# Performance work log

Measured on AMD Instinct MI355X. Metric: run time of the kernel, lower is better.

## Reference

```python
import jax, jax.numpy as jnp
import numpy as np

N, E, L, D, H = 20000, 100000, 4, 64, 8
HID = H * D  # LSTM hidden size = num_heads * out_dim


def setup_inputs() -> dict:
    key = jax.random.key(0)
    ks = jax.random.split(key, 8)
    s = 0.05
    return {
        "features": jax.random.normal(ks[0], (N, D), jnp.float32),
        "type_mask": jax.random.randint(ks[1], (N,), 0, 3),
        "edge_metapath_indices": jax.random.randint(ks[2], (E, L), 0, N),
        "dst": jax.random.randint(ks[3], (E,), 0, N),
        "W_ih": jax.random.normal(ks[4], (4 * HID, D), jnp.float32) * s,
        "W_hh": jax.random.normal(ks[5], (4 * HID, HID), jnp.float32) * s,
        "b_ih": jnp.zeros((4 * HID,), jnp.float32),
        "b_hh": jnp.zeros((4 * HID,), jnp.float32),
        "attn1_w": jax.random.normal(ks[6], (H, D), jnp.float32) * s,
        "attn2": jax.random.normal(ks[7], (1, H, D), jnp.float32) * s,
    }


def _lstm_last_hidden(x, W_ih, W_hh, b_ih, b_hh):
    # x: [L, E, D] time-major. PyTorch LSTM gate order: i, f, g, o.
    h0 = jnp.zeros((x.shape[1], W_hh.shape[1]), x.dtype)
    b = b_ih + b_hh

    def step(carry, xt):
        h, c = carry
        gates = xt @ W_ih.T + h @ W_hh.T + b  # [E, 4*HID]
        i, f, g, o = jnp.split(gates, 4, axis=-1)
        c = jax.nn.sigmoid(f) * c + jax.nn.sigmoid(i) * jnp.tanh(g)
        h = jax.nn.sigmoid(o) * jnp.tanh(c)
        return (h, c), None

    (h, _), _ = jax.lax.scan(step, (h0, h0), x)
    return h  # [E, HID]


def reference(features, type_mask, edge_metapath_indices, dst,
              W_ih, W_hh, b_ih, b_hh, attn1_w, attn2):
    alpha = 0.01  # LeakyReLU slope
    # gather metapath node features: [E, L, D]
    edata = features[edge_metapath_indices]
    h = _lstm_last_hidden(jnp.swapaxes(edata, 0, 1), W_ih, W_hh, b_ih, b_hh)
    eft = h.reshape(-1, H, D)  # [E, H, D]
    center = features[edge_metapath_indices[:, -1]]  # [E, D]
    a1 = center @ attn1_w.T                      # [E, H]
    a2 = jnp.sum(eft * attn2, axis=-1)           # [E, H]
    a = jax.nn.leaky_relu(a1 + a2, negative_slope=alpha)[:, :, None]  # [E, H, 1]
    # edge softmax: segmented by destination node
    amax = jax.ops.segment_max(a, dst, num_segments=N)
    amax = jnp.where(jnp.isfinite(amax), amax, 0.0)
    ex = jnp.exp(a - amax[dst])
    denom = jax.ops.segment_sum(ex, dst, num_segments=N)
    attn = ex / denom[dst]  # every edge's segment is nonempty
    # message passing: scatter-sum of eft * attn into dst nodes
    return jax.ops.segment_sum(eft * attn, dst, num_segments=N)  # [N, H, D]
```

## Files before the change

### kernel.cpp

```cpp
#include <hip/hip_runtime.h>
#include <hip/hip_bf16.h>
#include <stdint.h>

#define N_NODES 20000
#define E_EDGES 100000
#define L_SEQ   4
#define D_FEAT  64
#define H_HEADS 8
#define HID     512

typedef __attribute__((ext_vector_type(8))) short short8;
typedef __attribute__((ext_vector_type(4))) float floatx4;

__device__ __forceinline__ float sigmoidf_(float x) { return 1.0f / (1.0f + __expf(-x)); }
__device__ __forceinline__ float tanhf_(float x) {
    x = fminf(15.f, fmaxf(-15.f, x));
    float e = __expf(2.f * x);
    return (e - 1.f) / (e + 1.f);
}
__device__ __forceinline__ unsigned fkey(float f) {
    unsigned u = __float_as_uint(f);
    return (u & 0x80000000u) ? ~u : (u | 0x80000000u);
}
__device__ __forceinline__ float fdecode(unsigned k) {
    if (k == 0u) return 0.0f;
    unsigned u = (k & 0x80000000u) ? (k ^ 0x80000000u) : ~k;
    return __uint_as_float(u);
}
__device__ __forceinline__ short f2bf(float x) {
    __hip_bfloat16 b = __float2bfloat16(x);
    return *(short*)&b;
}
__device__ __forceinline__ float bf2f(short x) {
    __hip_bfloat16 b = *(__hip_bfloat16*)&x;
    return __bfloat162float(b);
}

__device__ __forceinline__ void gload16(const void* g, const void* l) {
    __builtin_amdgcn_global_load_lds(
        (const __attribute__((address_space(1))) unsigned int*)(uintptr_t)g,
        (__attribute__((address_space(3))) unsigned int*)(unsigned int)(uintptr_t)l,
        16, 0, 0);
}

__global__ __launch_bounds__(256) void feat2bf16(const float* __restrict__ f, short* __restrict__ fb) {
    int i = blockIdx.x * 256 + threadIdx.x;
    if (i < N_NODES * D_FEAT) fb[i] = f2bf(f[i]);
}

__global__ __launch_bounds__(128) void convert_weights(
    const float* __restrict__ W_ih, const float* __restrict__ W_hh,
    const float* __restrict__ b_ih, const float* __restrict__ b_hh,
    short* __restrict__ Wb_ih, short* __restrict__ Wb_hh, float* __restrict__ bias)
{
    int rp = blockIdx.x;
    int hblock = rp >> 7, rem = rp & 127;
    int half = (rem >> 6) & 1, gate = (rem >> 4) & 3, j = rem & 15;
    int ro = gate * HID + hblock * 32 + half * 16 + j;
    for (int k = threadIdx.x; k < D_FEAT; k += 128)
        Wb_ih[rp * D_FEAT + k] = f2bf(W_ih[ro * D_FEAT + k]);
    for (int k = threadIdx.x; k < HID; k += 128)
        Wb_hh[rp * HID + k] = f2bf(W_hh[ro * HID + k]);
    if (threadIdx.x == 0) bias[ro] = b_ih[ro] + b_hh[ro];
}

template <int FIRST>
__global__ __launch_bounds__(256) void lstm_mfma(
    const short* __restrict__ feats_bf,
    const int*   __restrict__ mp,
    const short* __restrict__ Wb_ih,
    const short* __restrict__ Wb_hh,
    const float* __restrict__ bias,
    const short* __restrict__ h_prev,
    short*       __restrict__ h_next,
    short*       __restrict__ c_state,
    int t, int cnt, int nslices)
{
    __shared__ __align__(16) short At[128 * 64];
    __shared__ __align__(16) short Bt[128 * 64];

    const int b     = blockIdx.x;
    const int xcd   = b & 7;
    const int slot  = b >> 3;
    const int g     = slot >> 4;
    const int bn    = slot & 15;
    const int slice = g * 8 + xcd;
    if (slice >= nslices) return;
    const int e0    = slice * 128;
    const int hb    = bn * 32;

    const int tid   = threadIdx.x;
    const int lane  = tid & 63;
    const int w     = tid >> 6;
    const int waveM = w & 1;
    const int waveN = w >> 1;
    const int quad  = lane >> 4;
    const int c16   = lane & 15;

    floatx4 acc[4][4];
#pragma unroll
    for (int a = 0; a < 4; ++a)
#pragma unroll
        for (int bb = 0; bb < 4; ++bb) acc[a][bb] = (floatx4){0.f, 0.f, 0.f, 0.f};

    const int nch = FIRST ? 1 : 9;
    for (int kc = 0; kc < nch; ++kc) {
#pragma unroll
        for (int i = 0; i < 4; ++i) {
            int sb = w * 256 + i * 64;
            int s  = sb + lane;
            int m  = s >> 3, p = s & 7;
            int pg = p ^ (m & 7);
            int e = e0 + m; if (e >= cnt) e = cnt - 1;
            const void* ga;
            if (kc == 0) {
                int row = mp[e * L_SEQ + t];
                ga = (const void*)(feats_bf + row * D_FEAT + pg * 8);
            } else {
                ga = (const void*)(h_prev + (size_t)e * HID + (kc - 1) * 64 + pg * 8);
            }
            gload16(ga, (const void*)&At[sb * 8]);
            int r = bn * 128 + m;
            const void* gb = (kc == 0)
                ? (const void*)(Wb_ih + r * D_FEAT + pg * 8)
                : (const void*)(Wb_hh + (size_t)r * HID + (kc - 1) * 64 + pg * 8);
            gload16(gb, (const void*)&Bt[sb * 8]);
        }
        __syncthreads();

#pragma unroll
        for (int ks = 0; ks < 2; ++ks) {
            short8 af[4], bfv[4];
#pragma unroll
            for (int mf = 0; mf < 4; ++mf) {
                int m  = waveM * 64 + mf * 16 + c16;
                int pw = ks * 4 + quad;
                af[mf] = *(const short8*)&At[m * 64 + ((pw ^ (m & 7)) * 8)];
            }
#pragma unroll
            for (int nf = 0; nf < 4; ++nf) {
                int n  = waveN * 64 + nf * 16 + c16;
                int pw = ks * 4 + quad;
                bfv[nf] = *(const short8*)&Bt[n * 64 + ((pw ^ (n & 7)) * 8)];
            }
#pragma unroll
            for (int mf = 0; mf < 4; ++mf)
#pragma unroll
                for (int nf = 0; nf < 4; ++nf)
                    acc[mf][nf] = __builtin_amdgcn_mfma_f32_16x16x32_bf16(
                        af[mf], bfv[nf], acc[mf][nf], 0, 0, 0);
        }
        __syncthreads();
    }

    const int n = hb + waveN * 16 + c16;
    const float bi  = bias[n];
    const float bff = bias[HID + n];
    const float bg  = bias[2 * HID + n];
    const float bo  = bias[3 * HID + n];
#pragma unroll
    for (int mf = 0; mf < 4; ++mf) {
#pragma unroll
        for (int r = 0; r < 4; ++r) {
            int e = e0 + waveM * 64 + mf * 16 + quad * 4 + r;
            if (e < cnt) {
                float gi = acc[mf][0][r] + bi;
                float gf = acc[mf][1][r] + bff;
                float gg = acc[mf][2][r] + bg;
                float go = acc[mf][3][r] + bo;
                float c_old = FIRST ? 0.f : bf2f(c_state[(size_t)e * HID + n]);
                float cn = sigmoidf_(gf) * c_old + sigmoidf_(gi) * tanhf_(gg);
                c_state[(size_t)e * HID + n] = f2bf(cn);
                h_next[(size_t)e * HID + n] = f2bf(sigmoidf_(go) * tanhf_(cn));
            }
        }
    }
}

__global__ __launch_bounds__(256) void attn_logits(
    const float* __restrict__ features,
    const int*   __restrict__ mp,
    const __hip_bfloat16* __restrict__ hfin,
    const float* __restrict__ attn1_w,
    const float* __restrict__ attn2,
    const int*   __restrict__ dst,
    float*       __restrict__ a_out,
    unsigned*    __restrict__ amax_key)
{
    const int e    = blockIdx.x * 4 + (threadIdx.x >> 6);
    const int lane = threadIdx.x & 63;
    const int ctr  = mp[e * L_SEQ + (L_SEQ - 1)];
    const float cd = features[ctr * D_FEAT + lane];
    const int dn   = dst[e];
#pragma unroll
    for (int h = 0; h < H_HEADS; ++h) {
        float v = cd * attn1_w[h * D_FEAT + lane]
                + __bfloat162float(hfin[(size_t)e * HID + h * D_FEAT + lane]) * attn2[h * D_FEAT + lane];
#pragma unroll
        for (int off = 32; off; off >>= 1) v += __shfl_xor(v, off, 64);
        if (lane == 0) {
            float lv = v > 0.f ? v : 0.01f * v;
            a_out[e * H_HEADS + h] = lv;
            atomicMax(&amax_key[dn * H_HEADS + h], fkey(lv));
        }
    }
}

__global__ __launch_bounds__(256) void exp_denom(
    const int*      __restrict__ dst,
    float*          __restrict__ a_out,
    const unsigned* __restrict__ amax_key,
    float*          __restrict__ denom)
{
    int i = blockIdx.x * 256 + threadIdx.x;
    if (i >= E_EDGES * H_HEADS) return;
    int e = i >> 3, h = i & 7;
    int dn = dst[e];
    float am = fdecode(amax_key[dn * H_HEADS + h]);
    float ex = __expf(a_out[i] - am);
    a_out[i] = ex;
    atomicAdd(&denom[dn * H_HEADS + h], ex);
}

__global__ __launch_bounds__(256) void scatter_out(
    const int*   __restrict__ dst,
    const float* __restrict__ a_out,
    const float* __restrict__ denom,
    const __hip_bfloat16* __restrict__ hfin,
    float*       __restrict__ out)
{
    const int e  = blockIdx.x;
    const int dn = dst[e];
    for (int j = threadIdx.x; j < HID; j += 256) {
        int h = j >> 6;
        float wgt = a_out[e * H_HEADS + h] / denom[dn * H_HEADS + h];
        atomicAdd(&out[(size_t)dn * HID + j], __bfloat162float(hfin[(size_t)e * HID + j]) * wgt);
    }
}

extern "C" void kernel_launch(void* const* d_in, const int* in_sizes, int n_in,
                              void* d_out, int out_size, void* d_ws, size_t ws_size,
                              hipStream_t stream) {
    const float* features = (const float*)d_in[0];
    const int*   mp       = (const int*)d_in[2];
    const int*   dst      = (const int*)d_in[3];
    const float* W_ih     = (const float*)d_in[4];
    const float* W_hh     = (const float*)d_in[5];
    const float* b_ih     = (const float*)d_in[6];
    const float* b_hh     = (const float*)d_in[7];
    const float* attn1_w  = (const float*)d_in[8];
    const float* attn2    = (const float*)d_in[9];
    float* out = (float*)d_out;

    char* ws = (char*)d_ws;
    size_t off = 0;
    float*    a_scr    = (float*)(ws + off); off += (size_t)E_EDGES * H_HEADS * sizeof(float);
    float*    denom    = (float*)(ws + off); off += (size_t)N_NODES * H_HEADS * sizeof(float);
    unsigned* amax_key = (unsigned*)(ws + off); off += (size_t)N_NODES * H_HEADS * sizeof(unsigned);
    short*    feats_bf = (short*)(ws + off); off += (size_t)N_NODES * D_FEAT * sizeof(short);
    short*    Wb_ih    = (short*)(ws + off); off += (size_t)4 * HID * D_FEAT * sizeof(short);
    short*    Wb_hh    = (short*)(ws + off); off += (size_t)4 * HID * HID * sizeof(short);
    float*    bias     = (float*)(ws + off); off += (size_t)4 * HID * sizeof(float);
    off = (off + 255) & ~(size_t)255;
    short*    eft      = (short*)(ws + off); off += (size_t)E_EDGES * HID * sizeof(short);
    off = (off + 255) & ~(size_t)255;

    const size_t per_edge = (size_t)HID * (2 + 2 + 2);
    size_t avail = (ws_size > off) ? (ws_size - off) : 0;
    long long cs_ll = ((long long)(avail / per_edge) / 1024) * 1024;
    int cs = (int)(cs_ll < 1024 ? 1024 : (cs_ll > E_EDGES ? E_EDGES : cs_ll));

    short* hA = (short*)(ws + off);
    short* hB = hA + (size_t)cs * HID;
    short* cS = hB + (size_t)cs * HID;

    hipMemsetAsync(d_out, 0, (size_t)out_size * sizeof(float), stream);
    hipMemsetAsync(denom, 0, (size_t)N_NODES * H_HEADS * sizeof(float), stream);
    hipMemsetAsync(amax_key, 0, (size_t)N_NODES * H_HEADS * sizeof(unsigned), stream);

    feat2bf16<<<(N_NODES * D_FEAT + 255) / 256, 256, 0, stream>>>(features, feats_bf);
    convert_weights<<<4 * HID, 128, 0, stream>>>(W_ih, W_hh, b_ih, b_hh, Wb_ih, Wb_hh, bias);

    for (int e0 = 0; e0 < E_EDGES; e0 += cs) {
        int cnt = E_EDGES - e0 < cs ? E_EDGES - e0 : cs;
        int nslices = (cnt + 127) / 128;
        int nslices_pad = (nslices + 7) & ~7;
        int nblk = nslices_pad * 16;
        const int* mpc = mp + (size_t)e0 * L_SEQ;
        short* eft_c = eft + (size_t)e0 * HID;
        lstm_mfma<1><<<nblk, 256, 0, stream>>>(feats_bf, mpc, Wb_ih, Wb_hh, bias, hA, hA, cS, 0, cnt, nslices);
        lstm_mfma<0><<<nblk, 256, 0, stream>>>(feats_bf, mpc, Wb_ih, Wb_hh, bias, hA, hB, cS, 1, cnt, nslices);
        lstm_mfma<0><<<nblk, 256, 0, stream>>>(feats_bf, mpc, Wb_ih, Wb_hh, bias, hB, hA, cS, 2, cnt, nslices);
        lstm_mfma<0><<<nblk, 256, 0, stream>>>(feats_bf, mpc, Wb_ih, Wb_hh, bias, hA, eft_c, cS, 3, cnt, nslices);
    }

    attn_logits<<<E_EDGES / 4, 256, 0, stream>>>(features, mp, (const __hip_bfloat16*)eft,
                                                 attn1_w, attn2, dst, a_scr, amax_key);
    exp_denom<<<(E_EDGES * H_HEADS + 255) / 256, 256, 0, stream>>>(dst, a_scr, amax_key, denom);
    scatter_out<<<E_EDGES, 256, 0, stream>>>(dst, a_scr, denom, (const __hip_bfloat16*)eft, out);
}
```

Measured before the change: 1.530 ms.

## Replace atomic edge-softmax scatter with CSR-based per-node gather

Builds a CSR index of edges grouped by destination (histogram, single-block scan, atomic fill), then computes the segment max, denominator and weighted sum per node in one gather kernel, dropping the global atomicMax/atomicAdd scatter passes and the output memset. The LSTM kernel is also restructured to hoist per-lane address computation and separate the input-projection chunk from the recurrent chunks with pointer increments. The CSR build adds several small serial launches, including a single-block scan, and edge order within a node is nondeterministic.

```diff
diff --git a/kernel.cpp b/kernel.cpp
--- a/kernel.cpp
+++ b/kernel.cpp
@@ -64,6 +64,47 @@
     if (threadIdx.x == 0) bias[ro] = b_ih[ro] + b_hh[ro];
 }
 
+__global__ __launch_bounds__(256) void deg_hist(const int* __restrict__ dst, int* __restrict__ deg) {
+    int i = blockIdx.x * 256 + threadIdx.x;
+    if (i < E_EDGES) atomicAdd(&deg[dst[i]], 1);
+}
+
+__global__ __launch_bounds__(1024) void scan_deg(const int* __restrict__ deg,
+                                                 int* __restrict__ row, int* __restrict__ cursor) {
+    __shared__ int buf[1024];
+    __shared__ int s_carry;
+    const int tid = threadIdx.x;
+    if (tid == 0) s_carry = 0;
+    __syncthreads();
+    for (int base = 0; base < N_NODES; base += 1024) {
+        int idx = base + tid;
+        int v = (idx < N_NODES) ? deg[idx] : 0;
+        buf[tid] = v;
+        __syncthreads();
+        for (int offd = 1; offd < 1024; offd <<= 1) {
+            int tv = (tid >= offd) ? buf[tid - offd] : 0;
+            __syncthreads();
+            buf[tid] += tv;
+            __syncthreads();
+        }
+        int c0 = s_carry;
+        if (idx < N_NODES) { row[idx] = c0 + buf[tid] - v; cursor[idx] = c0 + buf[tid] - v; }
+        __syncthreads();
+        if (tid == 1023) s_carry = c0 + buf[1023];
+        __syncthreads();
+    }
+    if (tid == 0) row[N_NODES] = s_carry;
+}
+
+__global__ __launch_bounds__(256) void fill_csr(const int* __restrict__ dst,
+                                                int* __restrict__ cursor, int* __restrict__ elist) {
+    int i = blockIdx.x * 256 + threadIdx.x;
+    if (i < E_EDGES) {
+        int p = atomicAdd(&cursor[dst[i]], 1);
+        elist[p] = i;
+    }
+}
+
 template <int FIRST>
 __global__ __launch_bounds__(256) void lstm_mfma(
     const short* __restrict__ feats_bf,
@@ -103,31 +144,18 @@
 #pragma unroll
         for (int bb = 0; bb < 4; ++bb) acc[a][bb] = (floatx4){0.f, 0.f, 0.f, 0.f};
 
-    const int nch = FIRST ? 1 : 9;
-    for (int kc = 0; kc < nch; ++kc) {
-#pragma unroll
-        for (int i = 0; i < 4; ++i) {
-            int sb = w * 256 + i * 64;
-            int s  = sb + lane;
-            int m  = s >> 3, p = s & 7;
-            int pg = p ^ (m & 7);
-            int e = e0 + m; if (e >= cnt) e = cnt - 1;
-            const void* ga;
-            if (kc == 0) {
-                int row = mp[e * L_SEQ + t];
-                ga = (const void*)(feats_bf + row * D_FEAT + pg * 8);
-            } else {
-                ga = (const void*)(h_prev + (size_t)e * HID + (kc - 1) * 64 + pg * 8);
-            }
-            gload16(ga, (const void*)&At[sb * 8]);
-            int r = bn * 128 + m;
-            const void* gb = (kc == 0)
-                ? (const void*)(Wb_ih + r * D_FEAT + pg * 8)
-                : (const void*)(Wb_hh + (size_t)r * HID + (kc - 1) * 64 + pg * 8);
-            gload16(gb, (const void*)&Bt[sb * 8]);
-        }
-        __syncthreads();
-
+    int eidx[4], mm[4], pgo[4];
+#pragma unroll
+    for (int i = 0; i < 4; ++i) {
+        int s = w * 256 + i * 64 + lane;
+        int m = s >> 3, p = s & 7;
+        pgo[i] = p ^ (m & 7);
+        mm[i]  = m;
+        int e  = e0 + m; if (e >= cnt) e = cnt - 1;
+        eidx[i] = e;
+    }
+
+    auto compute = [&]() {
 #pragma unroll
         for (int ks = 0; ks < 2; ++ks) {
             short8 af[4], bfv[4];
@@ -150,7 +178,37 @@
                     acc[mf][nf] = __builtin_amdgcn_mfma_f32_16x16x32_bf16(
                         af[mf], bfv[nf], acc[mf][nf], 0, 0, 0);
         }
-        __syncthreads();
+    };
+
+#pragma unroll
+    for (int i = 0; i < 4; ++i) {
+        int sb = w * 256 + i * 64;
+        int rowf = mp[eidx[i] * L_SEQ + t];
+        gload16((const void*)(feats_bf + rowf * D_FEAT + pgo[i] * 8), (const void*)&At[sb * 8]);
+        gload16((const void*)(Wb_ih + (bn * 128 + mm[i]) * D_FEAT + pgo[i] * 8), (const void*)&Bt[sb * 8]);
+    }
+    __syncthreads();
+    compute();
+
+    if (!FIRST) {
+        const short* ah[4]; const short* bh[4];
+#pragma unroll
+        for (int i = 0; i < 4; ++i) {
+            ah[i] = h_prev + (size_t)eidx[i] * HID + pgo[i] * 8;
+            bh[i] = Wb_hh + (size_t)(bn * 128 + mm[i]) * HID + pgo[i] * 8;
+        }
+        for (int kc = 1; kc <= 8; ++kc) {
+            __syncthreads();
+#pragma unroll
+            for (int i = 0; i < 4; ++i) {
+                int sb = w * 256 + i * 64;
+                gload16((const void*)ah[i], (const void*)&At[sb * 8]);
+                gload16((const void*)bh[i], (const void*)&Bt[sb * 8]);
+                ah[i] += 64; bh[i] += 64;
+            }
+            __syncthreads();
+            compute();
+        }
     }
 
     const int n = hb + waveN * 16 + c16;
@@ -183,15 +241,12 @@
     const __hip_bfloat16* __restrict__ hfin,
     const float* __restrict__ attn1_w,
     const float* __restrict__ attn2,
-    const int*   __restrict__ dst,
-    float*       __restrict__ a_out,
-    unsigned*    __restrict__ amax_key)
+    float*       __restrict__ a_out)
 {
     const int e    = blockIdx.x * 4 + (threadIdx.x >> 6);
     const int lane = threadIdx.x & 63;
     const int ctr  = mp[e * L_SEQ + (L_SEQ - 1)];
     const float cd = features[ctr * D_FEAT + lane];
-    const int dn   = dst[e];
 #pragma unroll
     for (int h = 0; h < H_HEADS; ++h) {
         float v = cd * attn1_w[h * D_FEAT + lane]
@@ -201,41 +256,70 @@
         if (lane == 0) {
             float lv = v > 0.f ? v : 0.01f * v;
             a_out[e * H_HEADS + h] = lv;
-            atomicMax(&amax_key[dn * H_HEADS + h], fkey(lv));
-        }
-    }
-}
-
-__global__ __launch_bounds__(256) void exp_denom(
-    const int*      __restrict__ dst,
-    float*          __restrict__ a_out,
-    const unsigned* __restrict__ amax_key,
-    float*          __restrict__ denom)
-{
-    int i = blockIdx.x * 256 + threadIdx.x;
-    if (i >= E_EDGES * H_HEADS) return;
-    int e = i >> 3, h = i & 7;
-    int dn = dst[e];
-    float am = fdecode(amax_key[dn * H_HEADS + h]);
-    float ex = __expf(a_out[i] - am);
-    a_out[i] = ex;
-    atomicAdd(&denom[dn * H_HEADS + h], ex);
-}
-
-__global__ __launch_bounds__(256) void scatter_out(
-    const int*   __restrict__ dst,
-    const float* __restrict__ a_out,
-    const float* __restrict__ denom,
-    const __hip_bfloat16* __restrict__ hfin,
+        }
+    }
+}
+
+__global__ __launch_bounds__(256) void gather_out(
+    const int*   __restrict__ row,
+    const int*   __restrict__ elist,
+    const float* __restrict__ a_scr,
+    const short* __restrict__ eft,
     float*       __restrict__ out)
 {
-    const int e  = blockIdx.x;
-    const int dn = dst[e];
-    for (int j = threadIdx.x; j < HID; j += 256) {
-        int h = j >> 6;
-        float wgt = a_out[e * H_HEADS + h] / denom[dn * H_HEADS + h];
-        atomicAdd(&out[(size_t)dn * HID + j], __bfloat162float(hfin[(size_t)e * HID + j]) * wgt);
-    }
+    const int n   = blockIdx.x;
+    const int tid = threadIdx.x;
+    const int beg = row[n];
+    const int deg = row[n + 1] - beg;
+    const int j0 = tid, j1 = tid + 256;
+
+    if (deg == 0) {
+        out[(size_t)n * HID + j0] = 0.f;
+        out[(size_t)n * HID + j1] = 0.f;
+        return;
+    }
+
+    __shared__ unsigned s_maxu[H_HEADS];
+    __shared__ float    s_max[H_HEADS];
+    __shared__ float    s_den[H_HEADS];
+    __shared__ float    s_w[128 * H_HEADS];
+    __shared__ int      s_e[128];
+
+    if (tid < H_HEADS) { s_maxu[tid] = 0u; s_den[tid] = 0.f; }
+    __syncthreads();
+    for (int i = tid; i < deg * H_HEADS; i += 256) {
+        int e = elist[beg + (i >> 3)], h = i & 7;
+        atomicMax(&s_maxu[h], fkey(a_scr[e * H_HEADS + h]));
+    }
+    __syncthreads();
+    if (tid < H_HEADS) s_max[tid] = fdecode(s_maxu[tid]);
+    __syncthreads();
+    for (int i = tid; i < deg * H_HEADS; i += 256) {
+        int e = elist[beg + (i >> 3)], h = i & 7;
+        atomicAdd(&s_den[h], __expf(a_scr[e * H_HEADS + h] - s_max[h]));
+    }
+    __syncthreads();
+
+    float acc0 = 0.f, acc1 = 0.f;
+    const int h0 = j0 >> 6, h1 = j1 >> 6;
+    for (int c0 = 0; c0 < deg; c0 += 128) {
+        int cc = min(128, deg - c0);
+        if (tid < cc) s_e[tid] = elist[beg + c0 + tid];
+        __syncthreads();
+        for (int i = tid; i < cc * H_HEADS; i += 256) {
+            int k = i >> 3, h = i & 7;
+            s_w[k * H_HEADS + h] = __expf(a_scr[s_e[k] * H_HEADS + h] - s_max[h]) / s_den[h];
+        }
+        __syncthreads();
+        for (int k = 0; k < cc; ++k) {
+            const short* er = eft + (size_t)s_e[k] * HID;
+            acc0 += s_w[k * H_HEADS + h0] * bf2f(er[j0]);
+            acc1 += s_w[k * H_HEADS + h1] * bf2f(er[j1]);
+        }
+        __syncthreads();
+    }
+    out[(size_t)n * HID + j0] = acc0;
+    out[(size_t)n * HID + j1] = acc1;
 }
 
 extern "C" void kernel_launch(void* const* d_in, const int* in_sizes, int n_in,
@@ -254,15 +338,17 @@
 
     char* ws = (char*)d_ws;
     size_t off = 0;
-    float*    a_scr    = (float*)(ws + off); off += (size_t)E_EDGES * H_HEADS * sizeof(float);
-    float*    denom    = (float*)(ws + off); off += (size_t)N_NODES * H_HEADS * sizeof(float);
-    unsigned* amax_key = (unsigned*)(ws + off); off += (size_t)N_NODES * H_HEADS * sizeof(unsigned);
-    short*    feats_bf = (short*)(ws + off); off += (size_t)N_NODES * D_FEAT * sizeof(short);
-    short*    Wb_ih    = (short*)(ws + off); off += (size_t)4 * HID * D_FEAT * sizeof(short);
-    short*    Wb_hh    = (short*)(ws + off); off += (size_t)4 * HID * HID * sizeof(short);
-    float*    bias     = (float*)(ws + off); off += (size_t)4 * HID * sizeof(float);
+    float* a_scr    = (float*)(ws + off); off += (size_t)E_EDGES * H_HEADS * sizeof(float);
+    int*   deg      = (int*)(ws + off);   off += (size_t)N_NODES * sizeof(int);
+    int*   row      = (int*)(ws + off);   off += ((size_t)N_NODES + 1) * sizeof(int);
+    int*   cursor   = (int*)(ws + off);   off += (size_t)N_NODES * sizeof(int);
+    int*   elist    = (int*)(ws + off);   off += (size_t)E_EDGES * sizeof(int);
+    short* feats_bf = (short*)(ws + off); off += (size_t)N_NODES * D_FEAT * sizeof(short);
+    short* Wb_ih    = (short*)(ws + off); off += (size_t)4 * HID * D_FEAT * sizeof(short);
+    short* Wb_hh    = (short*)(ws + off); off += (size_t)4 * HID * HID * sizeof(short);
+    float* bias     = (float*)(ws + off); off += (size_t)4 * HID * sizeof(float);
     off = (off + 255) & ~(size_t)255;
-    short*    eft      = (short*)(ws + off); off += (size_t)E_EDGES * HID * sizeof(short);
+    short* eft      = (short*)(ws + off); off += (size_t)E_EDGES * HID * sizeof(short);
     off = (off + 255) & ~(size_t)255;
 
     const size_t per_edge = (size_t)HID * (2 + 2 + 2);
@@ -274,9 +360,10 @@
     short* hB = hA + (size_t)cs * HID;
     short* cS = hB + (size_t)cs * HID;
 
-    hipMemsetAsync(d_out, 0, (size_t)out_size * sizeof(float), stream);
-    hipMemsetAsync(denom, 0, (size_t)N_NODES * H_HEADS * sizeof(float), stream);
-    hipMemsetAsync(amax_key, 0, (size_t)N_NODES * H_HEADS * sizeof(unsigned), stream);
+    hipMemsetAsync(deg, 0, (size_t)N_NODES * sizeof(int), stream);
+    deg_hist<<<(E_EDGES + 255) / 256, 256, 0, stream>>>(dst, deg);
+    scan_deg<<<1, 1024, 0, stream>>>(deg, row, cursor);
+    fill_csr<<<(E_EDGES + 255) / 256, 256, 0, stream>>>(dst, cursor, elist);
 
     feat2bf16<<<(N_NODES * D_FEAT + 255) / 256, 256, 0, stream>>>(features, feats_bf);
     convert_weights<<<4 * HID, 128, 0, stream>>>(W_ih, W_hh, b_ih, b_hh, Wb_ih, Wb_hh, bias);
@@ -295,7 +382,6 @@
     }
 
     attn_logits<<<E_EDGES / 4, 256, 0, stream>>>(features, mp, (const __hip_bfloat16*)eft,
-                                                 attn1_w, attn2, dst, a_scr, amax_key);
-    exp_denom<<<(E_EDGES * H_HEADS + 255) / 256, 256, 0, stream>>>(dst, a_scr, amax_key, denom);
-    scatter_out<<<E_EDGES, 256, 0, stream>>>(dst, a_scr, denom, (const __hip_bfloat16*)eft, out);
-}
+                                                 attn1_w, attn2, a_scr);
+    gather_out<<<N_NODES, 256, 0, stream>>>(row, elist, a_scr, eft, out);
+}
```

Result: faster. 1.476 ms (-3.5%).
